# Kernel optimization log

Measured on AMD Instinct MI355X. Metric: run time of the kernel, lower is better.

The kernel has to match this reference:

```python
import jax, jax.numpy as jnp
import numpy as np

B, S, H, E = 4, 2048, 1024, 8


def setup_inputs() -> dict:
    key = jax.random.key(0)
    k1, k2, k3 = jax.random.split(key, 3)
    scale = 1.0 / np.sqrt(H)
    return {
        "x": jax.random.normal(k1, (B, S, H), dtype=jnp.float32),
        "router_w": jax.random.normal(k2, (H, E), dtype=jnp.float32) * scale,
        "router_b": jnp.zeros((E,), dtype=jnp.float32),
        "expert_w": jax.random.normal(k3, (E, H, H), dtype=jnp.float32) * scale,
        "expert_b": jnp.zeros((E, H), dtype=jnp.float32),
    }


def reference(x, router_w, router_b, expert_w, expert_b):
    # Flatten tokens: [T, H]
    b, s, h = x.shape
    hs = x.reshape(-1, h)
    # Router: logits -> softmax -> top-1 expert (argmax), matching the
    # original forward which routes each token to argmax(softmax(logits)).
    logits = hs @ router_w + router_b                 # [T, E]
    probs = jax.nn.softmax(logits, axis=-1)           # [T, E]
    idx = jnp.argmax(probs, axis=-1)                  # [T]
    gate = jnp.take_along_axis(probs, idx[:, None], axis=-1)  # [T, 1]
    # Per-expert GEMM computed densely for all experts (reference baseline
    # for the sort/dispatch + grouped-GEMM kernel): [T, E, H]
    expert_out = jnp.einsum("th,ehd->ted", hs, expert_w) + expert_b
    # Combine: select routed expert's output, weight by gate value.
    dispatch = jax.nn.one_hot(idx, expert_w.shape[0], dtype=hs.dtype) * gate  # [T, E]
    out = jnp.einsum("te,ted->td", dispatch, expert_out)  # [T, H]
    return out.reshape(b, s, h)
```

## Files before the change

### kernel.cpp

```cpp
#include <hip/hip_runtime.h>

constexpr int kT = 8192;
constexpr int kH = 1024;
constexpr int kE = 8;
constexpr int kMaxTiles = 72;
constexpr int kCntStride = 32;

typedef short short8 __attribute__((ext_vector_type(8)));
typedef float floatx4 __attribute__((ext_vector_type(4)));

__device__ inline unsigned short f2b(float f) {
    union { float f; unsigned int u; } v; v.f = f;
    unsigned int r = v.u + 0x7FFFu + ((v.u >> 16) & 1u);
    return (unsigned short)(r >> 16);
}

#define GLDS16(gp, lp)                                                                  \
    __builtin_amdgcn_global_load_lds(                                                   \
        (const __attribute__((address_space(1))) unsigned int*)(gp),                    \
        (__attribute__((address_space(3))) unsigned int*)(lp), 16, 0, 0)

__global__ __launch_bounds__(256) void k_prep(const float* __restrict__ W,
                                              unsigned short* __restrict__ Wt,
                                              const float* __restrict__ x,
                                              unsigned short* __restrict__ xb,
                                              const float* __restrict__ rw,
                                              const float* __restrict__ rb,
                                              float* __restrict__ gate,
                                              int* __restrict__ idx,
                                              int* __restrict__ cnt,
                                              int* __restrict__ done) {
    __shared__ __align__(16) char smem[32768];
    int bid = blockIdx.x, tid = threadIdx.x;
    if (bid == 0 && tid < kE + 1) {
        if (tid < kE) cnt[tid * kCntStride] = 0; else *done = 0;
    }
    if (bid < 1024) {
        unsigned int* ldsw = (unsigned int*)smem;
        int tb = bid;
        int e = tb >> 7, kb = (tb >> 3) & 15, nb2 = tb & 7;
        const float* Wp = W + ((size_t)e << 20) + (size_t)(kb * 64) * kH + nb2 * 128;
        int c = (tid & 31) * 4;
        int rr = tid >> 5;
        unsigned int dw[4][4];
#pragma unroll
        for (int i = 0; i < 4; ++i) {
            int r0 = rr * 8 + i * 2;
            float4 v0 = *(const float4*)(Wp + (size_t)r0 * kH + c);
            float4 v1 = *(const float4*)(Wp + (size_t)(r0 + 1) * kH + c);
            dw[i][0] = (unsigned int)f2b(v0.x) | ((unsigned int)f2b(v1.x) << 16);
            dw[i][1] = (unsigned int)f2b(v0.y) | ((unsigned int)f2b(v1.y) << 16);
            dw[i][2] = (unsigned int)f2b(v0.z) | ((unsigned int)f2b(v1.z) << 16);
            dw[i][3] = (unsigned int)f2b(v0.w) | ((unsigned int)f2b(v1.w) << 16);
        }
#pragma unroll
        for (int j = 0; j < 4; ++j) {
            int n = c + j;
            int key = ((n ^ (n >> 3)) & 7) << 2;
            uint4 q{dw[0][j], dw[1][j], dw[2][j], dw[3][j]};
            *(uint4*)&ldsw[n * 32 + ((rr * 4) ^ key)] = q;
        }
        __syncthreads();
        unsigned short* Wo = Wt + ((size_t)e << 20) + (size_t)(nb2 * 128) * kH + kb * 64;
        int k8 = (tid & 7) * 8;
#pragma unroll
        for (int pp = 0; pp < 4; ++pp) {
            int n = pp * 32 + (tid >> 3);
            int key = ((n ^ (n >> 3)) & 7) << 2;
            uint4 q = *(const uint4*)&ldsw[n * 32 + (((tid & 7) * 4) ^ key)];
            *(uint4*)(Wo + (size_t)n * kH + k8) = q;
        }
        return;
    }
    float* rwlds = (float*)smem;
    int rid = bid - 1024;
#pragma unroll
    for (int i = 0; i < 8; ++i) {
        int g = i * 256 + tid;
        float4 v = *(const float4*)(rw + 4 * g);
        int pq = g ^ ((g >> 3) & 7);
        *(float4*)&rwlds[4 * pq] = v;
    }
    __syncthreads();
    int w = tid >> 6, lane = tid & 63;
    for (int tk = 0; tk < 2; ++tk) {
        int t = rid * 8 + w * 2 + tk;
        const float* xp = x + (size_t)t * kH;
        unsigned short* xop = xb + (size_t)t * kH;
        float pe[8];
#pragma unroll
        for (int e2 = 0; e2 < 8; ++e2) pe[e2] = 0.f;
#pragma unroll
        for (int j = 0; j < 4; ++j) {
            int h0 = j * 256 + lane * 4;
            float4 xv = *(const float4*)(xp + h0);
            ushort4 o;
            o.x = f2b(xv.x); o.y = f2b(xv.y); o.z = f2b(xv.z); o.w = f2b(xv.w);
            *(ushort4*)(xop + h0) = o;
            float xa[4] = {xv.x, xv.y, xv.z, xv.w};
#pragma unroll
            for (int cc = 0; cc < 4; ++cc) {
                int q0 = 2 * (h0 + cc);
                int key = (q0 >> 3) & 7;
                float4 w0 = *(const float4*)&rwlds[4 * (q0 ^ key)];
                float4 w1 = *(const float4*)&rwlds[4 * ((q0 + 1) ^ key)];
                float xs = xa[cc];
                pe[0] += xs * w0.x; pe[1] += xs * w0.y;
                pe[2] += xs * w0.z; pe[3] += xs * w0.w;
                pe[4] += xs * w1.x; pe[5] += xs * w1.y;
                pe[6] += xs * w1.z; pe[7] += xs * w1.w;
            }
        }
#pragma unroll
        for (int s = 1; s < 64; s <<= 1)
#pragma unroll
            for (int e2 = 0; e2 < 8; ++e2) pe[e2] += __shfl_xor(pe[e2], s);
        if (lane == 0) {
            float m = pe[0] + rb[0]; int bi = 0;
#pragma unroll
            for (int e2 = 1; e2 < 8; ++e2) {
                float l = pe[e2] + rb[e2];
                if (l > m) { m = l; bi = e2; }
            }
            float sum = 0.f;
#pragma unroll
            for (int e2 = 0; e2 < 8; ++e2) sum += __expf(pe[e2] + rb[e2] - m);
            gate[t] = 1.0f / sum;
            idx[t]  = bi;
        }
    }
}

__global__ __launch_bounds__(256) void k_rank(const int* __restrict__ idx,
                                              int* __restrict__ perm2,
                                              int* __restrict__ cnt,
                                              int* __restrict__ done,
                                              int* __restrict__ tile_e,
                                              int* __restrict__ tile_row) {
    __shared__ int lcnt[kE];
    __shared__ int lbase[kE];
    int tid = threadIdx.x;
    if (tid < kE) lcnt[tid] = 0;
    __syncthreads();
    int t = blockIdx.x * 256 + tid;
    int bi = idx[t];
    int lrank = atomicAdd(&lcnt[bi], 1);
    __syncthreads();
    if (tid < kE) lbase[tid] = atomicAdd(&cnt[tid * kCntStride], lcnt[tid]);
    __syncthreads();
    perm2[bi * kT + lbase[bi] + lrank] = t;
    __syncthreads();
    if (tid == 0) {
        __threadfence();
        int old = atomicAdd(done, 1);
        if (old == (int)gridDim.x - 1) {
            __threadfence();
            int tt = 0;
            for (int ee = 0; ee < kE; ++ee) {
                int c = atomicAdd(&cnt[ee * kCntStride], 0);
                int nt = (c + 127) >> 7;
                for (int i = 0; i < nt; ++i) { tile_e[tt] = ee; tile_row[tt] = i << 7; ++tt; }
            }
            for (; tt < kMaxTiles; ++tt) tile_e[tt] = -1;
        }
    }
}

constexpr int kBK = 64;

__global__ __launch_bounds__(256, 3) void k_gemm(const unsigned short* __restrict__ xb,
                                                 const unsigned short* __restrict__ Wt,
                                                 const float* __restrict__ eb,
                                                 const int* __restrict__ perm2,
                                                 const float* __restrict__ gate,
                                                 const int* __restrict__ cnt,
                                                 const int* __restrict__ tile_e,
                                                 const int* __restrict__ tile_row,
                                                 float* __restrict__ out) {
    int bm = blockIdx.x, bn = blockIdx.y;
    int e = tile_e[bm];
    if (e < 0) return;
    int l0 = tile_row[bm];
    int ce = cnt[e * kCntStride];
    const int* pe = perm2 + e * kT;

    __shared__ __align__(16) unsigned short As[128 * kBK];
    __shared__ __align__(16) unsigned short Bs[128 * kBK];

    int tid = threadIdx.x;
    int wave = tid >> 6, lane = tid & 63;
    int wm = wave & 1, wn = wave >> 1;
    int quad = lane >> 4, l15 = lane & 15;

    floatx4 acc[4][4];
#pragma unroll
    for (int i = 0; i < 4; ++i)
#pragma unroll
        for (int j = 0; j < 4; ++j) acc[i][j] = floatx4{0.f, 0.f, 0.f, 0.f};

    int lrow8 = lane >> 3;
    int lseg8 = (lane & 7) ^ lrow8;
    const unsigned short* aPj[4];
#pragma unroll
    for (int j = 0; j < 4; ++j) {
        int lr = l0 + wave * 32 + j * 8 + lrow8;
        int tok = (lr < ce) ? pe[lr] : 0;
        aPj[j] = xb + (size_t)tok * kH + lseg8 * 8;
    }
    const unsigned short* bP = Wt + ((size_t)e << 20)
                             + (size_t)(bn * 128 + wave * 32 + lrow8) * kH + lseg8 * 8;
    unsigned short* lA = &As[(wave * 32) * kBK];
    unsigned short* lB = &Bs[(wave * 32) * kBK];

    for (int k0 = 0; k0 < kH; k0 += kBK) {
        __syncthreads();
#pragma unroll
        for (int j = 0; j < 4; ++j) {
            GLDS16(aPj[j] + k0, lA + j * 8 * kBK);
            GLDS16(bP + (size_t)(j * 8) * kH + k0, lB + j * 8 * kBK);
        }
        __syncthreads();

#pragma unroll
        for (int ks = 0; ks < 2; ++ks) {
            int sw = ((ks * 4 + quad) ^ (l15 & 7)) * 8;
            short8 af[4], bf[4];
#pragma unroll
            for (int i = 0; i < 4; ++i)
                af[i] = *(const short8*)&As[(wm * 64 + i * 16 + l15) * kBK + sw];
#pragma unroll
            for (int j = 0; j < 4; ++j)
                bf[j] = *(const short8*)&Bs[(wn * 64 + j * 16 + l15) * kBK + sw];
#pragma unroll
            for (int i = 0; i < 4; ++i)
#pragma unroll
                for (int j = 0; j < 4; ++j)
                    acc[i][j] = __builtin_amdgcn_mfma_f32_16x16x32_bf16(af[i], bf[j],
                                                                        acc[i][j], 0, 0, 0);
        }
    }

    int colbase = bn * 128 + wn * 64;
#pragma unroll
    for (int i = 0; i < 4; ++i) {
        int rl = l0 + wm * 64 + i * 16 + quad * 4;
#pragma unroll
        for (int rg = 0; rg < 4; ++rg) {
            int lr = rl + rg;
            if (lr >= ce) continue;
            int tok = pe[lr];
            float g = gate[tok];
            float* op = out + (size_t)tok * kH;
#pragma unroll
            for (int j = 0; j < 4; ++j) {
                int col = colbase + j * 16 + l15;
                op[col] = g * (acc[i][j][rg] + eb[e * kH + col]);
            }
        }
    }
}

extern "C" void kernel_launch(void* const* d_in, const int* in_sizes, int n_in,
                              void* d_out, int out_size, void* d_ws, size_t ws_size,
                              hipStream_t stream) {
    const float* x  = (const float*)d_in[0];
    const float* rw = (const float*)d_in[1];
    const float* rb = (const float*)d_in[2];
    const float* ew = (const float*)d_in[3];
    const float* eb = (const float*)d_in[4];
    float* out = (float*)d_out;

    char* p = (char*)d_ws;
    unsigned short* Wt = (unsigned short*)p; p += (size_t)kE * kH * kH * 2;
    unsigned short* xb = (unsigned short*)p; p += (size_t)kT * kH * 2;
    float* gate  = (float*)p; p += (size_t)kT * 4;
    int* idx     = (int*)p;   p += (size_t)kT * 4;
    int* perm2   = (int*)p;   p += (size_t)kE * kT * 4;
    int* cnt     = (int*)p;   p += kE * kCntStride * 4;
    int* done    = (int*)p;   p += 64;
    int* tile_e  = (int*)p;   p += kMaxTiles * 4;
    int* tile_r  = (int*)p;   p += kMaxTiles * 4;

    k_prep<<<2048, 256, 0, stream>>>(ew, Wt, x, xb, rw, rb, gate, idx, cnt, done);
    k_rank<<<kT / 256, 256, 0, stream>>>(idx, perm2, cnt, done, tile_e, tile_r);
    dim3 gg(kMaxTiles, kH / 128);
    k_gemm<<<gg, 256, 0, stream>>>(xb, Wt, eb, perm2, gate, cnt, tile_e, tile_r, out);
}
```

Measured before the change: 156.3 us.

## Compute tile mapping in GEMM from counts and process two tokens per wave in router

The last-block tile-table construction in the rank kernel is removed: the atomic done counter, its threadfences and the serial loop that fills the table. Each GEMM block instead derives its expert and row offset by scanning the eight expert counts. Separately, the router part of the prep kernel has each half-wave handle one token, so a wave covers two tokens at once. This halves the number of router blocks and shortens the shuffle reduction to five steps. The cost is a redundant eight-entry count scan in every GEMM block.

```diff
diff --git a/kernel.cpp b/kernel.cpp
--- a/kernel.cpp
+++ b/kernel.cpp
@@ -28,13 +28,10 @@
                                               const float* __restrict__ rb,
                                               float* __restrict__ gate,
                                               int* __restrict__ idx,
-                                              int* __restrict__ cnt,
-                                              int* __restrict__ done) {
+                                              int* __restrict__ cnt) {
     __shared__ __align__(16) char smem[32768];
     int bid = blockIdx.x, tid = threadIdx.x;
-    if (bid == 0 && tid < kE + 1) {
-        if (tid < kE) cnt[tid * kCntStride] = 0; else *done = 0;
-    }
+    if (bid == 0 && tid < kE) cnt[tid * kCntStride] = 0;
     if (bid < 1024) {
         unsigned int* ldsw = (unsigned int*)smem;
         int tb = bid;
@@ -83,16 +80,17 @@
     }
     __syncthreads();
     int w = tid >> 6, lane = tid & 63;
-    for (int tk = 0; tk < 2; ++tk) {
-        int t = rid * 8 + w * 2 + tk;
+    int half = lane >> 5, l31 = lane & 31;
+    for (int tk2 = 0; tk2 < 2; ++tk2) {
+        int t = rid * 16 + w * 4 + tk2 * 2 + half;
         const float* xp = x + (size_t)t * kH;
         unsigned short* xop = xb + (size_t)t * kH;
         float pe[8];
 #pragma unroll
         for (int e2 = 0; e2 < 8; ++e2) pe[e2] = 0.f;
 #pragma unroll
-        for (int j = 0; j < 4; ++j) {
-            int h0 = j * 256 + lane * 4;
+        for (int j = 0; j < 8; ++j) {
+            int h0 = j * 128 + l31 * 4;
             float4 xv = *(const float4*)(xp + h0);
             ushort4 o;
             o.x = f2b(xv.x); o.y = f2b(xv.y); o.z = f2b(xv.z); o.w = f2b(xv.w);
@@ -112,10 +110,10 @@
             }
         }
 #pragma unroll
-        for (int s = 1; s < 64; s <<= 1)
+        for (int s = 1; s < 32; s <<= 1)
 #pragma unroll
             for (int e2 = 0; e2 < 8; ++e2) pe[e2] += __shfl_xor(pe[e2], s);
-        if (lane == 0) {
+        if (l31 == 0) {
             float m = pe[0] + rb[0]; int bi = 0;
 #pragma unroll
             for (int e2 = 1; e2 < 8; ++e2) {
@@ -133,10 +131,7 @@
 
 __global__ __launch_bounds__(256) void k_rank(const int* __restrict__ idx,
                                               int* __restrict__ perm2,
-                                              int* __restrict__ cnt,
-                                              int* __restrict__ done,
-                                              int* __restrict__ tile_e,
-                                              int* __restrict__ tile_row) {
+                                              int* __restrict__ cnt) {
     __shared__ int lcnt[kE];
     __shared__ int lbase[kE];
     int tid = threadIdx.x;
@@ -149,21 +144,6 @@
     if (tid < kE) lbase[tid] = atomicAdd(&cnt[tid * kCntStride], lcnt[tid]);
     __syncthreads();
     perm2[bi * kT + lbase[bi] + lrank] = t;
-    __syncthreads();
-    if (tid == 0) {
-        __threadfence();
-        int old = atomicAdd(done, 1);
-        if (old == (int)gridDim.x - 1) {
-            __threadfence();
-            int tt = 0;
-            for (int ee = 0; ee < kE; ++ee) {
-                int c = atomicAdd(&cnt[ee * kCntStride], 0);
-                int nt = (c + 127) >> 7;
-                for (int i = 0; i < nt; ++i) { tile_e[tt] = ee; tile_row[tt] = i << 7; ++tt; }
-            }
-            for (; tt < kMaxTiles; ++tt) tile_e[tt] = -1;
-        }
-    }
 }
 
 constexpr int kBK = 64;
@@ -174,14 +154,17 @@
                                                  const int* __restrict__ perm2,
                                                  const float* __restrict__ gate,
                                                  const int* __restrict__ cnt,
-                                                 const int* __restrict__ tile_e,
-                                                 const int* __restrict__ tile_row,
                                                  float* __restrict__ out) {
     int bm = blockIdx.x, bn = blockIdx.y;
-    int e = tile_e[bm];
+    int e = -1, l0 = 0, ce = 0, tilesum = 0;
+#pragma unroll
+    for (int ee = 0; ee < kE; ++ee) {
+        int c = cnt[ee * kCntStride];
+        int nt = (c + 127) >> 7;
+        if (e < 0 && bm < tilesum + nt) { e = ee; l0 = (bm - tilesum) << 7; ce = c; }
+        tilesum += nt;
+    }
     if (e < 0) return;
-    int l0 = tile_row[bm];
-    int ce = cnt[e * kCntStride];
     const int* pe = perm2 + e * kT;
 
     __shared__ __align__(16) unsigned short As[128 * kBK];
@@ -277,12 +260,9 @@
     int* idx     = (int*)p;   p += (size_t)kT * 4;
     int* perm2   = (int*)p;   p += (size_t)kE * kT * 4;
     int* cnt     = (int*)p;   p += kE * kCntStride * 4;
-    int* done    = (int*)p;   p += 64;
-    int* tile_e  = (int*)p;   p += kMaxTiles * 4;
-    int* tile_r  = (int*)p;   p += kMaxTiles * 4;
-
-    k_prep<<<2048, 256, 0, stream>>>(ew, Wt, x, xb, rw, rb, gate, idx, cnt, done);
-    k_rank<<<kT / 256, 256, 0, stream>>>(idx, perm2, cnt, done, tile_e, tile_r);
+
+    k_prep<<<1536, 256, 0, stream>>>(ew, Wt, x, xb, rw, rb, gate, idx, cnt);
+    k_rank<<<kT / 256, 256, 0, stream>>>(idx, perm2, cnt);
     dim3 gg(kMaxTiles, kH / 128);
-    k_gemm<<<gg, 256, 0, stream>>>(xb, Wt, eb, perm2, gate, cnt, tile_e, tile_r, out);
-}
+    k_gemm<<<gg, 256, 0, stream>>>(xb, Wt, eb, perm2, gate, cnt, out);
+}
```

Result: slower. 161.4 us (+3.3%).
